# Optimization experiments

Measured on AMD Instinct MI355X. Metric: run time of the kernel, lower is better.

Reference implementation:

```python
import jax, jax.numpy as jnp
import numpy as np

VOCAB = 256
EMBED = 1024
HIDDEN = 1024
LAYERS = 2
RATIO = 0.25
R_GATE = int(4 * HIDDEN * RATIO)   # low-rank dim of the 4H gate projection
R_DEC = int(VOCAB * RATIO)         # low-rank dim of decoder
BATCH, SEQ = 64, 256


def setup_inputs() -> dict:
    key = jax.random.key(0)
    ks = jax.random.split(key, 16)
    stdv = 1.0 / np.sqrt(HIDDEN)
    u = lambda k, shape, s: jax.random.uniform(k, shape, jnp.float32, -s, s)
    tokens = jax.random.randint(ks[0], (BATCH, SEQ), 0, VOCAB)
    embed = jax.random.normal(ks[1], (VOCAB, EMBED), jnp.float32)
    # per-layer low-rank LSTM params, stacked over layers (embed==hidden)
    VT_ih = u(ks[2], (LAYERS, R_GATE, HIDDEN), stdv)
    bVT_ih = u(ks[3], (LAYERS, R_GATE), stdv)
    U_ih = u(ks[4], (LAYERS, 4 * HIDDEN, R_GATE), stdv)
    bU_ih = u(ks[5], (LAYERS, 4 * HIDDEN), stdv)
    VT_hh = u(ks[6], (LAYERS, R_GATE, HIDDEN), stdv)
    bVT_hh = u(ks[7], (LAYERS, R_GATE), stdv)
    U_hh = u(ks[8], (LAYERS, 4 * HIDDEN, R_GATE), stdv)
    bU_hh = u(ks[9], (LAYERS, 4 * HIDDEN), stdv)
    # decoder LowRankLinear (nn.Linear default-ish init scale)
    s1 = 1.0 / np.sqrt(HIDDEN)
    s2 = 1.0 / np.sqrt(R_DEC)
    dec_VT = u(ks[10], (R_DEC, HIDDEN), s1)
    dec_bVT = u(ks[11], (R_DEC,), s1)
    dec_U = u(ks[12], (VOCAB, R_DEC), s2)
    dec_bU = u(ks[13], (VOCAB,), s2)
    return dict(tokens=tokens, embed=embed, VT_ih=VT_ih, bVT_ih=bVT_ih,
                U_ih=U_ih, bU_ih=bU_ih, VT_hh=VT_hh, bVT_hh=bVT_hh,
                U_hh=U_hh, bU_hh=bU_hh, dec_VT=dec_VT, dec_bVT=dec_bVT,
                dec_U=dec_U, dec_bU=dec_bU)


def _lstm_layer(x_seq, p):
    # x_seq: [T, B, H]; p: tuple of this layer's params
    vt_ih, bvt_ih, u_ih, bu_ih, vt_hh, bvt_hh, u_hh, bu_hh = p
    B = x_seq.shape[1]
    H = u_ih.shape[0] // 4
    h0 = jnp.zeros((B, H), x_seq.dtype)
    c0 = jnp.zeros((B, H), x_seq.dtype)

    def step(carry, x):
        h, c = carry
        gates = ((x @ vt_ih.T + bvt_ih) @ u_ih.T + bu_ih
                 + (h @ vt_hh.T + bvt_hh) @ u_hh.T + bu_hh)   # [B, 4H]
        i, f, g, o = jnp.split(gates, 4, axis=-1)
        i = jax.nn.sigmoid(i)
        f = jax.nn.sigmoid(f)
        g = jnp.tanh(g)
        o = jax.nn.sigmoid(o)
        c_new = f * c + i * g
        h_new = o * jnp.tanh(c_new)
        return (h_new, c_new), h_new

    _, out = jax.lax.scan(step, (h0, c0), x_seq)
    return out  # [T, B, H]


def reference(tokens, embed, VT_ih, bVT_ih, U_ih, bU_ih, VT_hh, bVT_hh,
              U_hh, bU_hh, dec_VT, dec_bVT, dec_U, dec_bU):
    x = embed[tokens]                 # [B, T, E]
    x = jnp.transpose(x, (1, 0, 2))   # time-major [T, B, E]
    for l in range(LAYERS):
        p = (VT_ih[l], bVT_ih[l], U_ih[l], bU_ih[l],
             VT_hh[l], bVT_hh[l], U_hh[l], bU_hh[l])
        x = _lstm_layer(x, p)
    # low-rank decoder: [T, B, H] -> [T, B, V]
    logits = (x @ dec_VT.T + dec_bVT) @ dec_U.T + dec_bU
    return jnp.transpose(logits, (1, 2, 0))  # [B, V, T]
```

## Files before the change

kernel.cpp:

```cpp
#include <hip/hip_runtime.h>
#include <hip/hip_bf16.h>


#define B_SZ   64
#define T_SEQ  256
#define HID    1024
#define G4     4096

typedef __attribute__((ext_vector_type(8))) short bf16x8;
typedef __attribute__((ext_vector_type(4))) float f32x4;
typedef __attribute__((ext_vector_type(4))) short bf16x4;
typedef unsigned long long u64;

__device__ __forceinline__ f32x4 mfma16(bf16x8 a, bf16x8 b, f32x4 c) {
  return __builtin_amdgcn_mfma_f32_16x16x32_bf16(a, b, c, 0, 0, 0);
}
__device__ __forceinline__ float sigm(float x)  { return 1.f / (1.f + __expf(-x)); }
__device__ __forceinline__ float tanh_(float x) { return 2.f / (1.f + __expf(-2.f * x)) - 1.f; }
__device__ __forceinline__ f32x4 fzero() { f32x4 z; z[0]=0.f; z[1]=0.f; z[2]=0.f; z[3]=0.f; return z; }

__device__ __forceinline__ bf16x8 lda(const __hip_bfloat16* p) {
  const u64* q = (const u64*)p;
  union { u64 u[2]; bf16x8 v; } r;
  r.u[0] = __hip_atomic_load(q,     __ATOMIC_RELAXED, __HIP_MEMORY_SCOPE_AGENT);
  r.u[1] = __hip_atomic_load(q + 1, __ATOMIC_RELAXED, __HIP_MEMORY_SCOPE_AGENT);
  return r.v;
}

__device__ __forceinline__ float ld1(const void* p, size_t i, int mode) {
  return mode ? ((const float*)p)[i]
              : __bfloat162float(((const __hip_bfloat16*)p)[i]);
}
__device__ __forceinline__ bf16x8 ld8(const void* p, size_t i, int mode) {
  if (mode) {
    const float* f = (const float*)p + i;
    float4 a = *(const float4*)f;
    float4 b = *(const float4*)(f + 4);
    union { bf16x8 v; __hip_bfloat16 h[8]; } u;
    u.h[0] = __float2bfloat16(a.x); u.h[1] = __float2bfloat16(a.y);
    u.h[2] = __float2bfloat16(a.z); u.h[3] = __float2bfloat16(a.w);
    u.h[4] = __float2bfloat16(b.x); u.h[5] = __float2bfloat16(b.y);
    u.h[6] = __float2bfloat16(b.z); u.h[7] = __float2bfloat16(b.w);
    return u.v;
  }
  return *(const bf16x8*)((const __hip_bfloat16*)p + i);
}

__global__ void k_detect(const unsigned short* __restrict__ e, int* __restrict__ flags) {
  __shared__ int cnt;
  if (threadIdx.x == 0) cnt = 0;
  __syncthreads();
  int c = 0;
  for (int i = threadIdx.x; i < 2048; i += 256) {
    unsigned int bits = ((unsigned int)e[2 * i]) << 16;
    float f = __uint_as_float(bits);
    if (!isfinite(f) || fabsf(f) > 1e10f) ++c;
  }
  atomicAdd(&cnt, c);
  __syncthreads();
  if (threadIdx.x == 0) flags[0] = (cnt > 8) ? 1 : 0;
}

__global__ void k_cvt_b(const void* __restrict__ src, __hip_bfloat16* __restrict__ dst,
                        int n, const int* __restrict__ flags) {
  const int mode = flags[0];
  for (int i = blockIdx.x * blockDim.x + threadIdx.x; i < n; i += gridDim.x * blockDim.x)
    dst[i] = mode ? __float2bfloat16(((const float*)src)[i])
                  : ((const __hip_bfloat16*)src)[i];
}
__global__ void k_cvt_f(const void* __restrict__ src, float* __restrict__ dst,
                        int n, const int* __restrict__ flags) {
  const int mode = flags[0];
  for (int i = blockIdx.x * blockDim.x + threadIdx.x; i < n; i += gridDim.x * blockDim.x)
    dst[i] = mode ? ((const float*)src)[i]
                  : __bfloat162float(((const __hip_bfloat16*)src)[i]);
}

__global__ void k_init(unsigned* bar) {
  bar[threadIdx.x] = 0u;
}

__global__ void __launch_bounds__(256) k_combine(
    const void* __restrict__ U_ih, const void* __restrict__ U_hh,
    const void* __restrict__ VT_ih, const void* __restrict__ VT_hh,
    __hip_bfloat16* __restrict__ Wc, const int* __restrict__ flags)
{
  __shared__ __hip_bfloat16 sB[4 * 64 * 8];
  const int mode = flags[0];
  const int idx  = blockIdx.x;
  const int Mid  = idx >> 10;
  const int rem  = idx & 1023;
  const int gblk = rem >> 4, kblk = rem & 15;
  const int L = Mid >> 1, typ = Mid & 1;
  const void* U  = typ ? U_hh  : U_ih;
  const void* VT = typ ? VT_hh : VT_ih;
  const size_t Uoff  = (size_t)L * G4 * HID;
  const size_t VToff = (size_t)L * HID * HID;
  const int tid = threadIdx.x, lane = tid & 63, wv = tid >> 6;

  f32x4 acc[4];
  for (int i = 0; i < 4; ++i) acc[i] = fzero();

  const int r_local = tid >> 3;
  const int kk8     = (tid & 7) * 8;

  for (int r0 = 0; r0 < HID; r0 += 32) {
    union { bf16x8 v; __hip_bfloat16 h[8]; } u;
    u.v = ld8(VT, VToff + (size_t)(r0 + r_local) * HID + kblk * 64 + kk8, mode);
    __syncthreads();
    #pragma unroll
    for (int j = 0; j < 8; ++j) {
      int k_local = kk8 + j;
      int tile = k_local >> 4;
      int ln   = ((r_local >> 3) << 4) | (k_local & 15);
      sB[(tile * 64 + ln) * 8 + (r_local & 7)] = u.h[j];
    }
    __syncthreads();
    bf16x8 a = ld8(U, Uoff + (size_t)(gblk * 64 + wv * 16 + (lane & 15)) * HID
                          + r0 + (lane >> 4) * 8, mode);
    #pragma unroll
    for (int nt = 0; nt < 4; ++nt) {
      bf16x8 b = *(const bf16x8*)(sB + (nt * 64 + lane) * 8);
      acc[nt] = mfma16(a, b, acc[nt]);
    }
  }
  #pragma unroll
  for (int nt = 0; nt < 4; ++nt)
    #pragma unroll
    for (int r = 0; r < 4; ++r) {
      int g = gblk * 64 + wv * 16 + (lane >> 4) * 4 + r;
      int k = kblk * 64 + nt * 16 + (lane & 15);
      Wc[((size_t)Mid * G4 + g) * HID + k] = __float2bfloat16(acc[nt][r]);
    }
}

__global__ void __launch_bounds__(256) k_bias(
    const void* __restrict__ bVT_ih, const void* __restrict__ U_ih,
    const void* __restrict__ bU_ih,
    const void* __restrict__ bVT_hh, const void* __restrict__ U_hh,
    const void* __restrict__ bU_hh,
    float* __restrict__ bc, const int* __restrict__ flags)
{
  const int mode  = flags[0];
  const int g_all = blockIdx.x * 4 + (threadIdx.x >> 6);
  const int lane  = threadIdx.x & 63;
  const int L = g_all >> 12, g = g_all & 4095;
  const size_t ub = (size_t)(L * G4 + g) * HID + lane * 16;
  const size_t vb = (size_t)L * HID + lane * 16;
  float s = 0.f;
  #pragma unroll
  for (int c = 0; c < 16; ++c)
    s += ld1(bVT_ih, vb + c, mode) * ld1(U_ih, ub + c, mode)
       + ld1(bVT_hh, vb + c, mode) * ld1(U_hh, ub + c, mode);
  for (int off = 32; off; off >>= 1) s += __shfl_down(s, off);
  if (lane == 0)
    bc[g_all] = s + ld1(bU_ih, L * G4 + g, mode) + ld1(bU_hh, L * G4 + g, mode);
}

__global__ void __launch_bounds__(256, 1) k_lstm(
    const int* __restrict__ tokens, const __hip_bfloat16* __restrict__ embedC,
    const __hip_bfloat16* __restrict__ Wc, const float* __restrict__ bc,
    __hip_bfloat16* __restrict__ H1, __hip_bfloat16* __restrict__ H2,
    unsigned* bar, const int h1mask, const int cmode)
{
  extern __shared__ char smem[];
  __hip_bfloat16* Wl = (__hip_bfloat16*)smem;
  f32x4* Xex = (f32x4*)(smem + 131072);
  __hip_bfloat16* Hs = (__hip_bfloat16*)(smem + 139264);

  const int tid  = threadIdx.x;
  const int lane = tid & 63, wv = tid >> 6;
  const int w    = blockIdx.x;
  const int L    = w >> 7, jg = w & 127;
  const int mat  = wv >> 1, mhalf = wv & 1;
  const u64* arr64 = (const u64*)bar;

  for (int q = tid; q < 8192; q += 256) {
    int m_ = q >> 12, ks = (q >> 7) & 31, tl = (q >> 6) & 1, ln = q & 63;
    int n_local = tl * 16 + (ln & 15);
    int g = (n_local >> 3) * 1024 + jg * 8 + (n_local & 7);
    int k = ks * 32 + (ln >> 4) * 8;
    *(bf16x8*)(Wl + (size_t)q * 8) =
        *(const bf16x8*)(Wc + (((size_t)(L * 2 + m_) * G4 + g) << 10) + k);
  }
  const int nb = lane & 7;
  const float b_i = bc[L * G4 +        jg * 8 + nb];
  const float b_f = bc[L * G4 + 1024 + jg * 8 + nb];
  const float b_g = bc[L * G4 + 2048 + jg * 8 + nb];
  const float b_o = bc[L * G4 + 3072 + jg * 8 + nb];
  __syncthreads();

  float cst[2][4] = {{0.f,0.f,0.f,0.f},{0.f,0.f,0.f,0.f}};
  const int m0 = mhalf * 32 + (lane & 15);
  const int ko = (lane >> 4) * 8;
  const __hip_bfloat16* wbase = Wl + mat * 32768;
  unsigned gen = 0;

  for (int s = 0; s <= T_SEQ; ++s) {
    const int t = s - L;
    const bool act = (t >= 0 && t < T_SEQ);
    if (act) {
      f32x4 acc00 = fzero(), acc01 = fzero(), acc10 = fzero(), acc11 = fzero();
      bool doGemm = true, cached = false;
      const __hip_bfloat16 *A0 = nullptr, *A1 = nullptr;
      if (mat == 0) {
        if (L == 0) {
          A0 = embedC + ((size_t)tokens[m0 * T_SEQ + t] << 10);
          A1 = embedC + ((size_t)tokens[(m0 + 16) * T_SEQ + t] << 10);
          cached = true;
        } else {
          A0 = H1 + ((((size_t)(t & h1mask)) * 64 + m0) << 10);
          A1 = A0 + ((size_t)16 << 10);
          cached = (cmode != 0);
        }
      } else {
        if (t == 0) doGemm = false;
        else {
          if (L == 0) {
            A0 = H1 + ((((size_t)((t - 1) & h1mask)) * 64 + m0) << 10);
            cached = (cmode != 0);
          } else {
            A0 = H2 + (((size_t)(t - 1) * 64 + m0) << 10);
            cached = true;
          }
          A1 = A0 + ((size_t)16 << 10);
        }
      }
      if (doGemm) {
        if (cached) {
          bf16x8 p0[32], p1[32];
          #pragma unroll
          for (int i = 0; i < 32; ++i) {
            p0[i] = *(const bf16x8*)(A0 + i * 32 + ko);
            p1[i] = *(const bf16x8*)(A1 + i * 32 + ko);
          }
          __builtin_amdgcn_sched_barrier(0);
          #pragma unroll
          for (int ks = 0; ks < 32; ++ks) {
            bf16x8 b0 = *(const bf16x8*)(wbase + (ks * 2 + 0) * 512 + lane * 8);
            bf16x8 b1 = *(const bf16x8*)(wbase + (ks * 2 + 1) * 512 + lane * 8);
            acc00 = mfma16(p0[ks], b0, acc00);
            acc01 = mfma16(p0[ks], b1, acc01);
            acc10 = mfma16(p1[ks], b0, acc10);
            acc11 = mfma16(p1[ks], b1, acc11);
          }
        } else {
          #pragma unroll 4
          for (int ks = 0; ks < 32; ++ks) {
            bf16x8 a0 = lda(A0 + ks * 32 + ko);
            bf16x8 a1 = lda(A1 + ks * 32 + ko);
            bf16x8 b0 = *(const bf16x8*)(wbase + (ks * 2 + 0) * 512 + lane * 8);
            bf16x8 b1 = *(const bf16x8*)(wbase + (ks * 2 + 1) * 512 + lane * 8);
            acc00 = mfma16(a0, b0, acc00);
            acc01 = mfma16(a0, b1, acc01);
            acc10 = mfma16(a1, b0, acc10);
            acc11 = mfma16(a1, b1, acc11);
          }
        }
      }
      if (mat == 0) {
        Xex[(mhalf * 4 + 0) * 64 + lane] = acc00;
        Xex[(mhalf * 4 + 1) * 64 + lane] = acc01;
        Xex[(mhalf * 4 + 2) * 64 + lane] = acc10;
        Xex[(mhalf * 4 + 3) * 64 + lane] = acc11;
      }
      __syncthreads();
      if (mat == 1) {
        #pragma unroll
        for (int mt = 0; mt < 2; ++mt) {
          f32x4 aT0 = mt ? acc10 : acc00;
          f32x4 aT1 = mt ? acc11 : acc01;
          f32x4 gx0 = Xex[(mhalf * 4 + mt * 2 + 0) * 64 + lane];
          f32x4 gx1 = Xex[(mhalf * 4 + mt * 2 + 1) * 64 + lane];
          #pragma unroll
          for (int r = 0; r < 4; ++r) {
            float v0 = aT0[r] + gx0[r];
            float v1 = aT1[r] + gx1[r];
            float p0 = __shfl_xor(v0, 8);
            float p1 = __shfl_xor(v1, 8);
            if ((lane & 15) < 8) {
              float iv = sigm(v0 + b_i);
              float fv = sigm(p0 + b_f);
              float gv = tanh_(v1 + b_g);
              float ov = sigm(p1 + b_o);
              float c  = fv * cst[mt][r] + iv * gv;
              cst[mt][r] = c;
              float h  = ov * tanh_(c);
              int m = mhalf * 32 + mt * 16 + (lane >> 4) * 4 + r;
              Hs[m * 8 + (lane & 15)] = __float2bfloat16(h);
            }
          }
        }
      }
      __syncthreads();
      if (tid < 128) {
        char* HoutB = (L == 0) ? (char*)(H1 + (((size_t)(t & h1mask)) << 16))
                               : (char*)(H2 + (((size_t)t) << 16));
        u64 v = ((const u64*)Hs)[tid];
        u64* dst = (u64*)(HoutB + ((size_t)(tid >> 1) << 11) + (jg << 4) + ((tid & 1) << 3));
        __hip_atomic_store(dst, v, __ATOMIC_RELAXED, __HIP_MEMORY_SCOPE_AGENT);
      }
    }
    __syncthreads();
    ++gen;
    if (wv == 0) {
      if (lane == 0)
        __hip_atomic_store(&bar[w], gen, __ATOMIC_RELAXED, __HIP_MEMORY_SCOPE_AGENT);
      for (;;) {
        u64 a = __hip_atomic_load(&arr64[2 * lane],     __ATOMIC_RELAXED, __HIP_MEMORY_SCOPE_AGENT);
        u64 b = __hip_atomic_load(&arr64[2 * lane + 1], __ATOMIC_RELAXED, __HIP_MEMORY_SCOPE_AGENT);
        bool ok = ((unsigned)a >= gen) && ((unsigned)(a >> 32) >= gen)
               && ((unsigned)b >= gen) && ((unsigned)(b >> 32) >= gen);
        if (__all(ok)) break;
        __builtin_amdgcn_s_sleep(2);
      }
    }
    __syncthreads();
  }
}

__global__ void __launch_bounds__(256) k_dec1(
    const __hip_bfloat16* __restrict__ H2, const __hip_bfloat16* __restrict__ dec_VTC,
    const float* __restrict__ dbv, __hip_bfloat16* __restrict__ R)
{
  const int t = blockIdx.x;
  const int lane = threadIdx.x & 63, wv = threadIdx.x >> 6;
  const __hip_bfloat16* A = H2 + ((size_t)t << 16) + ((size_t)(wv * 16 + (lane & 15)) << 10);
  const int ko = (lane >> 4) * 8;
  f32x4 acc[4];
  for (int i = 0; i < 4; ++i) acc[i] = fzero();
  for (int ks = 0; ks < 32; ++ks) {
    bf16x8 a = *(const bf16x8*)(A + ks * 32 + ko);
    #pragma unroll
    for (int nt = 0; nt < 4; ++nt) {
      bf16x8 b = *(const bf16x8*)(dec_VTC + ((size_t)(nt * 16 + (lane & 15)) << 10) + ks * 32 + ko);
      acc[nt] = mfma16(a, b, acc[nt]);
    }
  }
  #pragma unroll
  for (int nt = 0; nt < 4; ++nt) {
    int n = nt * 16 + (lane & 15);
    float bias = dbv[n];
    #pragma unroll
    for (int r = 0; r < 4; ++r) {
      int b_row = wv * 16 + (lane >> 4) * 4 + r;
      R[((size_t)t << 12) + (size_t)b_row * 64 + n] = __float2bfloat16(acc[nt][r] + bias);
    }
  }
}

__global__ void __launch_bounds__(256) k_dec2(
    const __hip_bfloat16* __restrict__ R, const __hip_bfloat16* __restrict__ dec_UC,
    const float* __restrict__ dbu, void* __restrict__ out,
    const int* __restrict__ flags)
{
  const int mode = flags[0];
  const int bblk = blockIdx.x >> 4, tblk = blockIdx.x & 15;
  const int lane = threadIdx.x & 63, wv = threadIdx.x >> 6;
  const int ko  = (lane >> 4) * 8;
  const int t_l = lane & 15;
  for (int bi = 0; bi < 4; ++bi) {
    const int b = bblk * 16 + wv * 4 + bi;
    f32x4 acc[16];
    for (int i = 0; i < 16; ++i) acc[i] = fzero();
    #pragma unroll
    for (int ks = 0; ks < 2; ++ks) {
      bf16x8 a = *(const bf16x8*)(R + (((size_t)(tblk * 16 + t_l) * 64 + b) << 6)
                                    + ks * 32 + ko);
      #pragma unroll
      for (int nt = 0; nt < 16; ++nt) {
        bf16x8 bb = *(const bf16x8*)(dec_UC + ((size_t)(nt * 16 + t_l) << 6) + ks * 32 + ko);
        acc[nt] = mfma16(a, bb, acc[nt]);
      }
    }
    #pragma unroll
    for (int nt = 0; nt < 16; ++nt) {
      int v = nt * 16 + t_l;
      float bias = dbu[v];
      size_t off = (size_t)b * 65536 + (size_t)v * 256 + tblk * 16 + (lane >> 4) * 4;
      if (mode) {
        float4 st;
        st.x = acc[nt][0] + bias; st.y = acc[nt][1] + bias;
        st.z = acc[nt][2] + bias; st.w = acc[nt][3] + bias;
        *(float4*)((float*)out + off) = st;
      } else {
        union { bf16x4 v4; __hip_bfloat16 h[4]; } u;
        #pragma unroll
        for (int r = 0; r < 4; ++r) u.h[r] = __float2bfloat16(acc[nt][r] + bias);
        *(bf16x4*)((__hip_bfloat16*)out + off) = u.v4;
      }
    }
  }
}

extern "C" void kernel_launch(void* const* d_in, const int* in_sizes, int n_in,
                              void* d_out, int out_size, void* d_ws, size_t ws_size,
                              hipStream_t stream)
{
  const int* tokens  = (const int*)d_in[0];
  const void* embed  = d_in[1];
  const void* VT_ih  = d_in[2];
  const void* bVT_ih = d_in[3];
  const void* U_ih   = d_in[4];
  const void* bU_ih  = d_in[5];
  const void* VT_hh  = d_in[6];
  const void* bVT_hh = d_in[7];
  const void* U_hh   = d_in[8];
  const void* bU_hh  = d_in[9];
  const void* dec_VT = d_in[10];
  const void* dec_bVT= d_in[11];
  const void* dec_U  = d_in[12];
  const void* dec_bU = d_in[13];

  char* ws = (char*)d_ws;
  const size_t M = 1024 * 1024;
  __hip_bfloat16* Wc      = (__hip_bfloat16*)ws;
  __hip_bfloat16* H2      = (__hip_bfloat16*)(ws + 32 * M);
  char* aux = ws + 64 * M;
  int*            flags   = (int*)aux;
  float*          bc      = (float*)(aux + 4096);
  float*          dbv     = (float*)(aux + 36864);
  float*          dbu     = (float*)(aux + 37120);
  __hip_bfloat16* embedC  = (__hip_bfloat16*)(aux + 65536);
  __hip_bfloat16* dec_VTC = (__hip_bfloat16*)(aux + 589824);
  __hip_bfloat16* dec_UC  = (__hip_bfloat16*)(aux + 720896);
  __hip_bfloat16* H1ring  = (__hip_bfloat16*)(aux + 1048576);
  unsigned*       bar     = (unsigned*)(aux + 1572864);
  __hip_bfloat16* R       = (__hip_bfloat16*)(aux + 2097152);
  __hip_bfloat16* H1big   = (__hip_bfloat16*)(ws + 68 * M);

  (void)in_sizes; (void)n_in; (void)out_size;

  const int big = (ws_size >= (size_t)100 * M);
  __hip_bfloat16* H1 = big ? H1big : H1ring;
  const int h1mask = big ? 255 : 3;
  const int cmode  = big ? 1 : 0;

  hipFuncSetAttribute((const void*)k_lstm,
                      hipFuncAttributeMaxDynamicSharedMemorySize, 140288);

  k_detect<<<1, 256, 0, stream>>>((const unsigned short*)embed, flags);
  k_cvt_b<<<256, 256, 0, stream>>>(embed,  embedC,  256 * 1024, flags);
  k_cvt_b<<<64,  256, 0, stream>>>(dec_VT, dec_VTC, 64 * 1024,  flags);
  k_cvt_b<<<16,  256, 0, stream>>>(dec_U,  dec_UC,  256 * 64,   flags);
  k_cvt_f<<<1,   64,  0, stream>>>(dec_bVT, dbv, 64,  flags);
  k_cvt_f<<<1,   256, 0, stream>>>(dec_bU,  dbu, 256, flags);
  k_combine<<<4096, 256, 0, stream>>>(U_ih, U_hh, VT_ih, VT_hh, Wc, flags);
  k_bias   <<<2048, 256, 0, stream>>>(bVT_ih, U_ih, bU_ih, bVT_hh, U_hh, bU_hh, bc, flags);
  k_init   <<<1, 256, 0, stream>>>(bar);
  k_lstm   <<<256, 256, 140288, stream>>>(tokens, embedC, Wc, bc, H1, H2, bar,
                                          h1mask, cmode);
  k_dec1   <<<256, 256, 0, stream>>>(H2, dec_VTC, dbv, R);
  k_dec2   <<<64, 256, 0, stream>>>(R, dec_UC, dbu, d_out, flags);
}
```

Measured before the change: 4.058 ms.

## Replace flat grid barrier with hierarchical two-level group barrier

Result: faster. 3.574 ms (-11.9%).

```diff
diff --git a/kernel.cpp b/kernel.cpp
--- a/kernel.cpp
+++ b/kernel.cpp
@@ -77,7 +77,7 @@
 }
 
 __global__ void k_init(unsigned* bar) {
-  bar[threadIdx.x] = 0u;
+  for (int i = threadIdx.x; i < 1024; i += 256) bar[i] = 0u;
 }
 
 __global__ void __launch_bounds__(256) k_combine(
@@ -173,7 +173,6 @@
   const int w    = blockIdx.x;
   const int L    = w >> 7, jg = w & 127;
   const int mat  = wv >> 1, mhalf = wv & 1;
-  const u64* arr64 = (const u64*)bar;
 
   for (int q = tid; q < 8192; q += 256) {
     int m_ = q >> 12, ks = (q >> 7) & 31, tl = (q >> 6) & 1, ln = q & 63;
@@ -195,6 +194,9 @@
   const int ko = (lane >> 4) * 8;
   const __hip_bfloat16* wbase = Wl + mat * 32768;
   unsigned gen = 0;
+
+  const int bg   = w & 7;
+  const int bsub = w >> 3;
 
   for (int s = 0; s <= T_SEQ; ++s) {
     const int t = s - L;
@@ -305,14 +307,40 @@
     ++gen;
     if (wv == 0) {
       if (lane == 0)
-        __hip_atomic_store(&bar[w], gen, __ATOMIC_RELAXED, __HIP_MEMORY_SCOPE_AGENT);
-      for (;;) {
-        u64 a = __hip_atomic_load(&arr64[2 * lane],     __ATOMIC_RELAXED, __HIP_MEMORY_SCOPE_AGENT);
-        u64 b = __hip_atomic_load(&arr64[2 * lane + 1], __ATOMIC_RELAXED, __HIP_MEMORY_SCOPE_AGENT);
-        bool ok = ((unsigned)a >= gen) && ((unsigned)(a >> 32) >= gen)
-               && ((unsigned)b >= gen) && ((unsigned)(b >> 32) >= gen);
-        if (__all(ok)) break;
-        __builtin_amdgcn_s_sleep(2);
+        __hip_atomic_store(&bar[bg * 32 + bsub], gen,
+                           __ATOMIC_RELAXED, __HIP_MEMORY_SCOPE_AGENT);
+      if (bsub == 0) {
+        const u64* gs = (const u64*)(bar + bg * 32);
+        const int li = lane & 15;
+        for (;;) {
+          u64 v = __hip_atomic_load(&gs[li], __ATOMIC_RELAXED, __HIP_MEMORY_SCOPE_AGENT);
+          bool ok = ((unsigned)v >= gen) && ((unsigned)(v >> 32) >= gen);
+          if (__all(ok)) break;
+          __builtin_amdgcn_s_sleep(1);
+        }
+        if (lane == 0)
+          __hip_atomic_store(&bar[256 + bg], gen,
+                             __ATOMIC_RELAXED, __HIP_MEMORY_SCOPE_AGENT);
+        const u64* rf = (const u64*)(bar + 256);
+        const int ri = lane & 3;
+        for (;;) {
+          u64 v = __hip_atomic_load(&rf[ri], __ATOMIC_RELAXED, __HIP_MEMORY_SCOPE_AGENT);
+          bool ok = ((unsigned)v >= gen) && ((unsigned)(v >> 32) >= gen);
+          if (__all(ok)) break;
+          __builtin_amdgcn_s_sleep(1);
+        }
+        if (lane == 0)
+          __hip_atomic_store(&bar[512 + bg * 16], gen,
+                             __ATOMIC_RELAXED, __HIP_MEMORY_SCOPE_AGENT);
+      } else {
+        if (lane == 0) {
+          for (;;) {
+            unsigned v = __hip_atomic_load(&bar[512 + bg * 16],
+                                           __ATOMIC_RELAXED, __HIP_MEMORY_SCOPE_AGENT);
+            if (v >= gen) break;
+            __builtin_amdgcn_s_sleep(2);
+          }
+        }
       }
     }
     __syncthreads();
```

## Replace global all-block barrier with per-layer leader-based dependency flags

Applied to the files above, without the earlier changes.

Measured after the change: 3.288 ms. 1.23x faster.

```diff
diff --git a/kernel.cpp b/kernel.cpp
--- a/kernel.cpp
+++ b/kernel.cpp
@@ -77,7 +77,7 @@
 }
 
 __global__ void k_init(unsigned* bar) {
-  bar[threadIdx.x] = 0u;
+  for (int i = threadIdx.x; i < 1024; i += 256) bar[i] = 0u;
 }
 
 __global__ void __launch_bounds__(256) k_combine(
@@ -173,7 +173,7 @@
   const int w    = blockIdx.x;
   const int L    = w >> 7, jg = w & 127;
   const int mat  = wv >> 1, mhalf = wv & 1;
-  const u64* arr64 = (const u64*)bar;
+  const bool leaderWave = (jg == 0) && (wv == 0);
 
   for (int q = tid; q < 8192; q += 256) {
     int m_ = q >> 12, ks = (q >> 7) & 31, tl = (q >> 6) & 1, ln = q & 63;
@@ -194,128 +194,144 @@
   const int m0 = mhalf * 32 + (lane & 15);
   const int ko = (lane >> 4) * 8;
   const __hip_bfloat16* wbase = Wl + mat * 32768;
-  unsigned gen = 0;
-
-  for (int s = 0; s <= T_SEQ; ++s) {
-    const int t = s - L;
-    const bool act = (t >= 0 && t < T_SEQ);
-    if (act) {
-      f32x4 acc00 = fzero(), acc01 = fzero(), acc10 = fzero(), acc11 = fzero();
-      bool doGemm = true, cached = false;
-      const __hip_bfloat16 *A0 = nullptr, *A1 = nullptr;
-      if (mat == 0) {
+  unsigned* Xrel = bar + 256 + L * 128;
+
+  for (int t = 0; t < T_SEQ; ++t) {
+    if (leaderWave) {
+      const u64* own = (const u64*)bar + (L ? 64 : 0);
+      const u64* oth = (const u64*)bar + (L ? 0 : 64);
+      const unsigned need = (unsigned)t;
+      for (;;) {
+        u64 a = __hip_atomic_load(&own[lane], __ATOMIC_RELAXED, __HIP_MEMORY_SCOPE_AGENT);
+        bool ok = ((unsigned)a >= need) && ((unsigned)(a >> 32) >= need);
+        if (L == 1) {
+          u64 b = __hip_atomic_load(&oth[lane], __ATOMIC_RELAXED, __HIP_MEMORY_SCOPE_AGENT);
+          ok = ok && ((unsigned)b >= need + 1) && ((unsigned)(b >> 32) >= need + 1);
+        } else if (cmode == 0) {
+          u64 b = __hip_atomic_load(&oth[lane], __ATOMIC_RELAXED, __HIP_MEMORY_SCOPE_AGENT);
+          ok = ok && ((unsigned)b + 3u >= need) && ((unsigned)(b >> 32) + 3u >= need);
+        }
+        if (__all(ok)) break;
+        __builtin_amdgcn_s_sleep(1);
+      }
+      if (lane < 8)
+        __hip_atomic_store(&Xrel[lane * 16], (unsigned)(t + 1),
+                           __ATOMIC_RELAXED, __HIP_MEMORY_SCOPE_AGENT);
+    } else if (L == 1 || mat == 1) {
+      if (lane == 0) {
+        for (;;) {
+          unsigned v = __hip_atomic_load(&Xrel[(w & 7) * 16],
+                                         __ATOMIC_RELAXED, __HIP_MEMORY_SCOPE_AGENT);
+          if (v >= (unsigned)(t + 1)) break;
+          __builtin_amdgcn_s_sleep(2);
+        }
+      }
+    }
+
+    f32x4 acc00 = fzero(), acc01 = fzero(), acc10 = fzero(), acc11 = fzero();
+    bool doGemm = true, cached = false;
+    const __hip_bfloat16 *A0 = nullptr, *A1 = nullptr;
+    if (mat == 0) {
+      if (L == 0) {
+        A0 = embedC + ((size_t)tokens[m0 * T_SEQ + t] << 10);
+        A1 = embedC + ((size_t)tokens[(m0 + 16) * T_SEQ + t] << 10);
+        cached = true;
+      } else {
+        A0 = H1 + ((((size_t)(t & h1mask)) * 64 + m0) << 10);
+        A1 = A0 + ((size_t)16 << 10);
+        cached = (cmode != 0);
+      }
+    } else {
+      if (t == 0) doGemm = false;
+      else {
         if (L == 0) {
-          A0 = embedC + ((size_t)tokens[m0 * T_SEQ + t] << 10);
-          A1 = embedC + ((size_t)tokens[(m0 + 16) * T_SEQ + t] << 10);
+          A0 = H1 + ((((size_t)((t - 1) & h1mask)) * 64 + m0) << 10);
+          cached = (cmode != 0);
+        } else {
+          A0 = H2 + (((size_t)(t - 1) * 64 + m0) << 10);
           cached = true;
-        } else {
-          A0 = H1 + ((((size_t)(t & h1mask)) * 64 + m0) << 10);
-          A1 = A0 + ((size_t)16 << 10);
-          cached = (cmode != 0);
+        }
+        A1 = A0 + ((size_t)16 << 10);
+      }
+    }
+    if (doGemm) {
+      if (cached) {
+        bf16x8 p0[32], p1[32];
+        #pragma unroll
+        for (int i = 0; i < 32; ++i) {
+          p0[i] = *(const bf16x8*)(A0 + i * 32 + ko);
+          p1[i] = *(const bf16x8*)(A1 + i * 32 + ko);
+        }
+        __builtin_amdgcn_sched_barrier(0);
+        #pragma unroll
+        for (int ks = 0; ks < 32; ++ks) {
+          bf16x8 b0 = *(const bf16x8*)(wbase + (ks * 2 + 0) * 512 + lane * 8);
+          bf16x8 b1 = *(const bf16x8*)(wbase + (ks * 2 + 1) * 512 + lane * 8);
+          acc00 = mfma16(p0[ks], b0, acc00);
+          acc01 = mfma16(p0[ks], b1, acc01);
+          acc10 = mfma16(p1[ks], b0, acc10);
+          acc11 = mfma16(p1[ks], b1, acc11);
         }
       } else {
-        if (t == 0) doGemm = false;
-        else {
-          if (L == 0) {
-            A0 = H1 + ((((size_t)((t - 1) & h1mask)) * 64 + m0) << 10);
-            cached = (cmode != 0);
-          } else {
-            A0 = H2 + (((size_t)(t - 1) * 64 + m0) << 10);
-            cached = true;
+        #pragma unroll 4
+        for (int ks = 0; ks < 32; ++ks) {
+          bf16x8 a0 = lda(A0 + ks * 32 + ko);
+          bf16x8 a1 = lda(A1 + ks * 32 + ko);
+          bf16x8 b0 = *(const bf16x8*)(wbase + (ks * 2 + 0) * 512 + lane * 8);
+          bf16x8 b1 = *(const bf16x8*)(wbase + (ks * 2 + 1) * 512 + lane * 8);
+          acc00 = mfma16(a0, b0, acc00);
+          acc01 = mfma16(a0, b1, acc01);
+          acc10 = mfma16(a1, b0, acc10);
+          acc11 = mfma16(a1, b1, acc11);
+        }
+      }
+    }
+    if (mat == 0) {
+      Xex[(mhalf * 4 + 0) * 64 + lane] = acc00;
+      Xex[(mhalf * 4 + 1) * 64 + lane] = acc01;
+      Xex[(mhalf * 4 + 2) * 64 + lane] = acc10;
+      Xex[(mhalf * 4 + 3) * 64 + lane] = acc11;
+    }
+    __syncthreads();
+    if (mat == 1) {
+      #pragma unroll
+      for (int mt = 0; mt < 2; ++mt) {
+        f32x4 aT0 = mt ? acc10 : acc00;
+        f32x4 aT1 = mt ? acc11 : acc01;
+        f32x4 gx0 = Xex[(mhalf * 4 + mt * 2 + 0) * 64 + lane];
+        f32x4 gx1 = Xex[(mhalf * 4 + mt * 2 + 1) * 64 + lane];
+        #pragma unroll
+        for (int r = 0; r < 4; ++r) {
+          float v0 = aT0[r] + gx0[r];
+          float v1 = aT1[r] + gx1[r];
+          float p0 = __shfl_xor(v0, 8);
+          float p1 = __shfl_xor(v1, 8);
+          if ((lane & 15) < 8) {
+            float iv = sigm(v0 + b_i);
+            float fv = sigm(p0 + b_f);
+            float gv = tanh_(v1 + b_g);
+            float ov = sigm(p1 + b_o);
+            float c  = fv * cst[mt][r] + iv * gv;
+            cst[mt][r] = c;
+            float h  = ov * tanh_(c);
+            int m = mhalf * 32 + mt * 16 + (lane >> 4) * 4 + r;
+            Hs[m * 8 + (lane & 15)] = __float2bfloat16(h);
           }
-          A1 = A0 + ((size_t)16 << 10);
-        }
-      }
-      if (doGemm) {
-        if (cached) {
-          bf16x8 p0[32], p1[32];
-          #pragma unroll
-          for (int i = 0; i < 32; ++i) {
-            p0[i] = *(const bf16x8*)(A0 + i * 32 + ko);
-            p1[i] = *(const bf16x8*)(A1 + i * 32 + ko);
-          }
-          __builtin_amdgcn_sched_barrier(0);
-          #pragma unroll
-          for (int ks = 0; ks < 32; ++ks) {
-            bf16x8 b0 = *(const bf16x8*)(wbase + (ks * 2 + 0) * 512 + lane * 8);
-            bf16x8 b1 = *(const bf16x8*)(wbase + (ks * 2 + 1) * 512 + lane * 8);
-            acc00 = mfma16(p0[ks], b0, acc00);
-            acc01 = mfma16(p0[ks], b1, acc01);
-            acc10 = mfma16(p1[ks], b0, acc10);
-            acc11 = mfma16(p1[ks], b1, acc11);
-          }
-        } else {
-          #pragma unroll 4
-          for (int ks = 0; ks < 32; ++ks) {
-            bf16x8 a0 = lda(A0 + ks * 32 + ko);
-            bf16x8 a1 = lda(A1 + ks * 32 + ko);
-            bf16x8 b0 = *(const bf16x8*)(wbase + (ks * 2 + 0) * 512 + lane * 8);
-            bf16x8 b1 = *(const bf16x8*)(wbase + (ks * 2 + 1) * 512 + lane * 8);
-            acc00 = mfma16(a0, b0, acc00);
-            acc01 = mfma16(a0, b1, acc01);
-            acc10 = mfma16(a1, b0, acc10);
-            acc11 = mfma16(a1, b1, acc11);
-          }
-        }
-      }
-      if (mat == 0) {
-        Xex[(mhalf * 4 + 0) * 64 + lane] = acc00;
-        Xex[(mhalf * 4 + 1) * 64 + lane] = acc01;
-        Xex[(mhalf * 4 + 2) * 64 + lane] = acc10;
-        Xex[(mhalf * 4 + 3) * 64 + lane] = acc11;
-      }
-      __syncthreads();
-      if (mat == 1) {
-        #pragma unroll
-        for (int mt = 0; mt < 2; ++mt) {
-          f32x4 aT0 = mt ? acc10 : acc00;
-          f32x4 aT1 = mt ? acc11 : acc01;
-          f32x4 gx0 = Xex[(mhalf * 4 + mt * 2 + 0) * 64 + lane];
-          f32x4 gx1 = Xex[(mhalf * 4 + mt * 2 + 1) * 64 + lane];
-          #pragma unroll
-          for (int r = 0; r < 4; ++r) {
-            float v0 = aT0[r] + gx0[r];
-            float v1 = aT1[r] + gx1[r];
-            float p0 = __shfl_xor(v0, 8);
-            float p1 = __shfl_xor(v1, 8);
-            if ((lane & 15) < 8) {
-              float iv = sigm(v0 + b_i);
-              float fv = sigm(p0 + b_f);
-              float gv = tanh_(v1 + b_g);
-              float ov = sigm(p1 + b_o);
-              float c  = fv * cst[mt][r] + iv * gv;
-              cst[mt][r] = c;
-              float h  = ov * tanh_(c);
-              int m = mhalf * 32 + mt * 16 + (lane >> 4) * 4 + r;
-              Hs[m * 8 + (lane & 15)] = __float2bfloat16(h);
-            }
-          }
-        }
-      }
-      __syncthreads();
-      if (tid < 128) {
-        char* HoutB = (L == 0) ? (char*)(H1 + (((size_t)(t & h1mask)) << 16))
-                               : (char*)(H2 + (((size_t)t) << 16));
-        u64 v = ((const u64*)Hs)[tid];
-        u64* dst = (u64*)(HoutB + ((size_t)(tid >> 1) << 11) + (jg << 4) + ((tid & 1) << 3));
-        __hip_atomic_store(dst, v, __ATOMIC_RELAXED, __HIP_MEMORY_SCOPE_AGENT);
+        }
       }
     }
     __syncthreads();
-    ++gen;
-    if (wv == 0) {
-      if (lane == 0)
-        __hip_atomic_store(&bar[w], gen, __ATOMIC_RELAXED, __HIP_MEMORY_SCOPE_AGENT);
-      for (;;) {
-        u64 a = __hip_atomic_load(&arr64[2 * lane],     __ATOMIC_RELAXED, __HIP_MEMORY_SCOPE_AGENT);
-        u64 b = __hip_atomic_load(&arr64[2 * lane + 1], __ATOMIC_RELAXED, __HIP_MEMORY_SCOPE_AGENT);
-        bool ok = ((unsigned)a >= gen) && ((unsigned)(a >> 32) >= gen)
-               && ((unsigned)b >= gen) && ((unsigned)(b >> 32) >= gen);
-        if (__all(ok)) break;
-        __builtin_amdgcn_s_sleep(2);
-      }
+    if (tid < 128) {
+      char* HoutB = (L == 0) ? (char*)(H1 + (((size_t)(t & h1mask)) << 16))
+                             : (char*)(H2 + (((size_t)t) << 16));
+      u64 v = ((const u64*)Hs)[tid];
+      u64* dst = (u64*)(HoutB + ((size_t)(tid >> 1) << 11) + (jg << 4) + ((tid & 1) << 3));
+      __hip_atomic_store(dst, v, __ATOMIC_RELAXED, __HIP_MEMORY_SCOPE_AGENT);
     }
     __syncthreads();
+    if (wv == 0 && lane == 0)
+      __hip_atomic_store(&bar[w], (unsigned)(t + 1),
+                         __ATOMIC_RELAXED, __HIP_MEMORY_SCOPE_AGENT);
   }
 }
 
```
